# Kernel tuning notes

Measured on AMD Instinct MI355X. Metric: run time of the kernel, lower is better.

## Reference

```python
import jax, jax.numpy as jnp
import numpy as np
from jax import lax

RADII = (0.1, 0.2, 0.4)
NSAMPLES = (16, 32, 128)
MLPS = ((3, 32, 32, 64), (3, 64, 64, 128), (3, 64, 96, 128))  # divide_ratio=1


def fps(xyz, npoint):
    # iterative farthest point sampling; xyz [B,N,3] -> idx [B,npoint]
    B, N, _ = xyz.shape
    def body(carry, _):
        mind, last = carry
        p = jnp.take_along_axis(xyz, last[:, None, None], axis=1)  # [B,1,3]
        d = jnp.sum((xyz - p) ** 2, -1)
        mind = jnp.minimum(mind, d)
        nxt = jnp.argmax(mind, -1).astype(jnp.int32)
        return (mind, nxt), last
    init = (jnp.full((B, N), 1e10, xyz.dtype), jnp.zeros((B,), jnp.int32))
    _, idx = lax.scan(body, init, None, length=npoint)
    return jnp.transpose(idx)  # [B,npoint]


def ball_query(radius, nsample, xyz, new_xyz):
    # first-nsample neighbors within radius; pad with first valid index
    N = xyz.shape[1]
    sq = jnp.sum((new_xyz[:, :, None, :] - xyz[:, None, :, :]) ** 2, -1)  # [B,S,N]
    cand = jnp.where(sq < radius * radius,
                     jnp.arange(N, dtype=jnp.int32)[None, None, :], N)
    idx = jnp.sort(cand, axis=-1)[:, :, :nsample]
    first = idx[:, :, :1]
    return jnp.where(idx == N, first, idx).astype(jnp.int32)


def scale_branch(xyz, new_xyz, radius, nsample, weights):
    idx = ball_query(radius, nsample, xyz, new_xyz)
    grouped = jax.vmap(lambda x, i: x[i])(xyz, idx)          # [B,S,ns,3]
    h = grouped - new_xyz[:, :, None, :]                      # relative coords (points=None)
    for w, b in weights:                                      # shared 1x1-conv MLP
        h = jax.nn.relu(jnp.einsum('bsnc,co->bsno', h, w) + b)
    return jnp.max(h, axis=2)                                 # maxpool over neighbors [B,S,C]


def _forward(pcd, params, wf, bf):
    npoint = pcd.shape[1] // 8
    idx = fps(pcd, npoint)
    new_xyz = jnp.take_along_axis(pcd, idx[:, :, None], axis=1)  # [B,S,3]
    feats = [scale_branch(pcd, new_xyz, RADII[i], NSAMPLES[i], params[i]) for i in range(3)]
    h = jnp.concatenate(feats, axis=-1)                          # [B,S,320]
    return jnp.einsum('bsc,co->bso', h, wf) + bf                 # patch values [B,S,1]


def setup_inputs() -> dict:
    key = jax.random.key(0)
    ks = jax.random.split(key, 32)
    B, N = 8, 4096
    inp = {"pcd": jax.random.uniform(ks[0], (B, N, 3), jnp.float32)}
    ki = 1
    for si, dims in enumerate(MLPS):
        for li in range(3):
            cin, cout = dims[li], dims[li + 1]
            inp[f"w{si}{li}"] = jax.random.normal(ks[ki], (cin, cout), jnp.float32) * (2.0 / cin) ** 0.5
            inp[f"b{si}{li}"] = jnp.zeros((cout,), jnp.float32)
            ki += 1
    inp["wf"] = jax.random.normal(ks[ki], (320, 1), jnp.float32) * 0.05
    inp["bf"] = jnp.zeros((1,), jnp.float32)
    return inp


def reference(pcd, w00, b00, w01, b01, w02, b02,
              w10, b10, w11, b11, w12, b12,
              w20, b20, w21, b21, w22, b22, wf, bf):
    params = [[(w00, b00), (w01, b01), (w02, b02)],
              [(w10, b10), (w11, b11), (w12, b12)],
              [(w20, b20), (w21, b21), (w22, b22)]]
    return _forward(pcd, params, wf, bf)
```

## Files before the change

### kernel.cpp

```cpp
#include <hip/hip_runtime.h>

#define BATCH 8
#define NPTS 4096
#define NSAMP 512

#define ROW_SHR(n) (0x110 | (n))
#define ROW_BCAST15 0x142
#define ROW_BCAST31 0x143

template <int CTRL, int RMASK>
__device__ __forceinline__ float fmax_dpp(float x) {
  int t = __builtin_amdgcn_update_dpp(0, __float_as_int(x), CTRL, RMASK, 0xf, true);
  return fmaxf(x, __int_as_float(t));
}

__device__ __forceinline__ float wave_max(float x) {
  x = fmax_dpp<ROW_SHR(1), 0xf>(x);
  x = fmax_dpp<ROW_SHR(2), 0xf>(x);
  x = fmax_dpp<ROW_SHR(4), 0xf>(x);
  x = fmax_dpp<ROW_SHR(8), 0xf>(x);
  x = fmax_dpp<ROW_BCAST15, 0xa>(x);
  x = fmax_dpp<ROW_BCAST31, 0xc>(x);
  return x;
}

__device__ __forceinline__ void tsec(int g, const float* __restrict__ w,
                                     float* __restrict__ wt, int cin, int cinp,
                                     int cout, int base) {
  int local = g - base;
  if (local < 0 || local >= cinp * cout) return;
  int oc = local / cinp, ic = local % cinp;
  wt[base + local] = (ic < cin) ? w[ic * cout + oc] : 0.0f;
}

__device__ __forceinline__ void rowpack(int g, const float* __restrict__ w20,
                                        const float* __restrict__ b20,
                                        const float* __restrict__ w21,
                                        float* __restrict__ wt, int base) {
  int local = g - base;
  if (local < 0 || local >= 4 * 64 * 32) return;
  int wq = local / (64 * 32);
  int r = local % (64 * 32);
  int k = r / 32, j = r % 32;
  float v;
  if (j < 3) v = w20[j * 64 + k];
  else if (j == 3) v = b20[k];
  else if (j < 28) v = w21[k * 96 + wq * 24 + (j - 4)];
  else v = 0.0f;
  wt[base + local] = v;
}

#define W00 0
#define W01 128
#define W02 1152
#define W10 3200
#define W11 3456
#define W12 7552
#define WROW 15744
#define W22V 23936
#define WT_TOTAL 36224

__global__ __launch_bounds__(256) void prep_kernel(
    const float* w00, const float* w01, const float* w02,
    const float* w10, const float* w11, const float* w12,
    const float* w20, const float* b20, const float* w21, const float* w22,
    float* __restrict__ wt) {
  int g = blockIdx.x * 256 + threadIdx.x;
  tsec(g, w00, wt, 3, 4, 32, W00);
  tsec(g, w01, wt, 32, 32, 32, W01);
  tsec(g, w02, wt, 32, 32, 64, W02);
  tsec(g, w10, wt, 3, 4, 64, W10);
  tsec(g, w11, wt, 64, 64, 64, W11);
  tsec(g, w12, wt, 64, 64, 128, W12);
  rowpack(g, w20, b20, w21, wt, WROW);
  tsec(g, w22, wt, 96, 96, 128, W22V);
}

template <int TOC, int TN>
__device__ __forceinline__ void ib(float (&acc)[TOC][TN], const float* bias) {
#pragma unroll
  for (int j = 0; j < TOC; ++j) {
    float bj = bias[j];
#pragma unroll
    for (int i = 0; i < TN; ++i) acc[j][i] = bj;
  }
}

template <int CIN4, int TOC, int TN, int NTPI, int WS>
__device__ __forceinline__ void layer_acc(const float* __restrict__ wtb,
                                          const float* hin,
                                          float (&acc)[TOC][TN], int tn) {
#pragma unroll 2
  for (int c4 = 0; c4 < CIN4; ++c4) {
    float hv[4][TN];
#pragma unroll
    for (int k = 0; k < 4; ++k) {
      const float* src = &hin[(c4 * 4 + k) * NTPI + tn * TN];
      if constexpr (TN == 1) {
        hv[k][0] = src[0];
      } else if constexpr (TN == 2) {
        float2 v = *(const float2*)src; hv[k][0] = v.x; hv[k][1] = v.y;
      } else {
        float4 v = *(const float4*)src;
        hv[k][0] = v.x; hv[k][1] = v.y; hv[k][2] = v.z; hv[k][3] = v.w;
      }
    }
#pragma unroll
    for (int j = 0; j < TOC; ++j) {
      float4 w4 = *(const float4*)&wtb[j * WS + c4 * 4];
#pragma unroll
      for (int i = 0; i < TN; ++i) {
        acc[j][i] = fmaf(hv[0][i], w4.x, acc[j][i]);
        acc[j][i] = fmaf(hv[1][i], w4.y, acc[j][i]);
        acc[j][i] = fmaf(hv[2][i], w4.z, acc[j][i]);
        acc[j][i] = fmaf(hv[3][i], w4.w, acc[j][i]);
      }
    }
  }
}

template <int TOC, int TN, int NTPO>
__device__ __forceinline__ void store_relu(float* hout,
                                           float (&acc)[TOC][TN], int tn) {
#pragma unroll
  for (int j = 0; j < TOC; ++j) {
    float* dst = &hout[j * NTPO + tn * TN];
    if constexpr (TN == 1) {
      dst[0] = fmaxf(acc[j][0], 0.0f);
    } else if constexpr (TN == 2) {
      *(float2*)dst = make_float2(fmaxf(acc[j][0], 0.0f),
                                  fmaxf(acc[j][1], 0.0f));
    } else {
      *(float4*)dst = make_float4(fmaxf(acc[j][0], 0.0f),
                                  fmaxf(acc[j][1], 0.0f),
                                  fmaxf(acc[j][2], 0.0f),
                                  fmaxf(acc[j][3], 0.0f));
    }
  }
}

template <int TOC, int TN>
__device__ __forceinline__ void rmax_upd(float (&r)[TOC],
                                         float (&acc)[TOC][TN]) {
#pragma unroll
  for (int j = 0; j < TOC; ++j) {
    float m = 0.0f;
#pragma unroll
    for (int i = 0; i < TN; ++i) m = fmaxf(m, acc[j][i]);
    r[j] = fmaxf(r[j], m);
  }
}

template <int TOC, int TN>
__device__ __forceinline__ float rmax_dot(const float* wfp,
                                          float (&acc)[TOC][TN], int tn) {
  float s = 0.0f;
#pragma unroll
  for (int j = 0; j < TOC; ++j) {
    float v = 0.0f;
#pragma unroll
    for (int i = 0; i < TN; ++i) v = fmaxf(v, acc[j][i]);
    v = fmaxf(v, __shfl_xor(v, 1));
    v = fmaxf(v, __shfl_xor(v, 2));
    v = fmaxf(v, __shfl_xor(v, 4));
    v = fmaxf(v, __shfl_xor(v, 8));
    if (tn == 0) s = fmaf(v, wfp[j], s);
  }
  return s;
}

__global__ __launch_bounds__(256) void fused_kernel(
    const float* __restrict__ pcd, float* __restrict__ new_xyz,
    int* __restrict__ ctrl, const float* __restrict__ wt,
    const float* __restrict__ b00, const float* __restrict__ b01,
    const float* __restrict__ b02, const float* __restrict__ b10,
    const float* __restrict__ b11, const float* __restrict__ b12,
    const float* __restrict__ b21, const float* __restrict__ b22,
    const float* __restrict__ wf, const float* __restrict__ bf,
    float* __restrict__ out) {
  __shared__ __align__(16) float lds[6160];

  const int tid = threadIdx.x;
  int* progress = ctrl + 8;

  if (tid == 0) ((int*)lds)[0] = atomicAdd(&ctrl[0], 1);
  __syncthreads();
  const int ticket = ((int*)lds)[0];

  if (ticket < BATCH) {
    const int b = ticket;
    const int t = tid;
    const int wave = t >> 6, lane = t & 63;
    const float* xb = pcd + (size_t)b * NPTS * 3;
    float4* slot = (float4*)(lds + 16);

    float X[16], Y[16], Z[16], mind[16];
    {
      float f[48];
      float4* vv = (float4*)f;
      const float4* src = (const float4*)xb + t * 12;
#pragma unroll
      for (int q = 0; q < 12; ++q) vv[q] = src[q];
#pragma unroll
      for (int j = 0; j < 16; ++j) {
        X[j] = f[3 * j + 0]; Y[j] = f[3 * j + 1]; Z[j] = f[3 * j + 2];
        mind[j] = 10000000000.0f;
      }
    }
    float px = xb[0], py = xb[1], pz = xb[2];

    for (int it = 0; it < NSAMP; ++it) {
      if (t == 0) {
        int* dst = (int*)(new_xyz + ((size_t)b * NSAMP + it) * 3);
        atomicExch(&dst[0], __float_as_int(px));
        atomicExch(&dst[1], __float_as_int(py));
        atomicExch(&dst[2], __float_as_int(pz));
        if ((it & 7) == 7)
          __hip_atomic_store(&progress[b], it + 1, __ATOMIC_RELEASE,
                             __HIP_MEMORY_SCOPE_AGENT);
      }
      float bv = -1.0f, bx = 0.0f, by = 0.0f, bz = 0.0f;
#pragma unroll
      for (int j = 0; j < 16; ++j) {
        float dx = __fsub_rn(X[j], px);
        float dy = __fsub_rn(Y[j], py);
        float dz = __fsub_rn(Z[j], pz);
        float d = __fadd_rn(__fadd_rn(__fmul_rn(dx, dx), __fmul_rn(dy, dy)),
                            __fmul_rn(dz, dz));
        float m = fminf(mind[j], d);
        mind[j] = m;
        bool g = m > bv;
        bv = g ? m : bv;
        bx = g ? X[j] : bx; by = g ? Y[j] : by; bz = g ? Z[j] : bz;
      }
      float wmax = __int_as_float(
          __builtin_amdgcn_readlane(__float_as_int(wave_max(bv)), 63));
      unsigned long long msk = __ballot(bv == wmax);
      if (lane == __ffsll(msk) - 1)
        slot[(it & 1) * 4 + wave] = make_float4(bx, by, bz, wmax);
      __syncthreads();
      float4 cur = slot[(it & 1) * 4 + 0];
#pragma unroll
      for (int w = 1; w < 4; ++w) {
        float4 sw = slot[(it & 1) * 4 + w];
        if (sw.w > cur.w) cur = sw;
      }
      px = cur.x; py = cur.y; pz = cur.z;
    }
    return;
  }

  const int tk = ticket - BATCH;
  const int b = tk & 7;
  const int s = tk >> 3;
  const int bs = (b << 9) | s;
  const int lane = tid & 63;
  const int wave = tid >> 6;
  const int tn = tid & 15, toc = tid >> 4;
  const float* xb = pcd + (size_t)b * NPTS * 3;

  float* bc = lds + 4;
  float* wsum = lds + 8;
  float* h2 = lds + 16;
  unsigned long long* masks = (unsigned long long*)(lds + 16);
  unsigned short* gl = (unsigned short*)(lds + 400);
  float* cbuf = lds + 488;
  float* sB = lds + 760;
  float* sA = lds + 2936;

  if (tid == 0) {
    while (__hip_atomic_load(&progress[b], __ATOMIC_ACQUIRE,
                             __HIP_MEMORY_SCOPE_AGENT) <= s)
      __builtin_amdgcn_s_sleep(2);
    const int* src = (const int*)(new_xyz + (size_t)bs * 3);
    bc[0] = __int_as_float(__hip_atomic_load(&src[0], __ATOMIC_RELAXED,
                                             __HIP_MEMORY_SCOPE_AGENT));
    bc[1] = __int_as_float(__hip_atomic_load(&src[1], __ATOMIC_RELAXED,
                                             __HIP_MEMORY_SCOPE_AGENT));
    bc[2] = __int_as_float(__hip_atomic_load(&src[2], __ATOMIC_RELAXED,
                                             __HIP_MEMORY_SCOPE_AGENT));
  }
  __syncthreads();
  const float cx = bc[0], cy = bc[1], cz = bc[2];

  const float r2a = (float)(0.1 * 0.1);
  const float r2b = (float)(0.2 * 0.2);
  const float r2c = (float)(0.4 * 0.4);
#pragma unroll 4
  for (int j = 0; j < 16; ++j) {
    int i = (j << 8) | tid;
    const float* p = xb + i * 3;
    float dx = __fsub_rn(cx, p[0]);
    float dy = __fsub_rn(cy, p[1]);
    float dz = __fsub_rn(cz, p[2]);
    float sq = __fadd_rn(__fadd_rn(__fmul_rn(dx, dx), __fmul_rn(dy, dy)),
                         __fmul_rn(dz, dz));
    unsigned long long m0 = __ballot(sq < r2a);
    unsigned long long m1 = __ballot(sq < r2b);
    unsigned long long m2 = __ballot(sq < r2c);
    if (lane == 0) {
      int c = (j << 2) | wave;
      masks[0 * 64 + c] = m0; masks[1 * 64 + c] = m1; masks[2 * 64 + c] = m2;
    }
  }
  __syncthreads();

  if (wave < 3) {
    const int ns  = (wave == 0) ? 16 : (wave == 1) ? 32 : 128;
    const int off = (wave == 0) ? 0  : (wave == 1) ? 16 : 48;
    unsigned long long m = masks[wave * 64 + lane];
    int pc = (int)__popcll(m);
    int incl = pc;
#pragma unroll
    for (int o = 1; o < 64; o <<= 1) {
      int u = __shfl_up(incl, o);
      if (lane >= o) incl += u;
    }
    int ex = incl - pc;
    int total = __shfl(incl, 63);
    unsigned short* glw = gl + off;
    unsigned long long mm = m;
    int p = ex;
    while (mm && p < ns) {
      int l = (int)__builtin_ctzll(mm);
      mm &= mm - 1;
      glw[p++] = (unsigned short)((lane << 6) | l);
    }
    int cnt = total < ns ? total : ns;
    unsigned long long nz = __ballot(pc > 0);
    int fl = __ffsll(nz) - 1;
    int myf = (lane << 6) | (int)__builtin_ctzll(m | 0x8000000000000000ull);
    int fidx = __shfl(myf, fl);
    for (int k = cnt + lane; k < ns; k += 64) glw[k] = (unsigned short)fidx;
  }
  __syncthreads();

  const int gi0 = gl[48 + lane];
  const int gi1 = gl[112 + lane];
  if (tid < 68) cbuf[3 * 68 + tid] = 0.0f;
  if (tid < 48) {
    int j = gl[tid];
    const float* p = xb + 3 * j;
    cbuf[0 * 68 + tid] = __fsub_rn(p[0], cx);
    cbuf[1 * 68 + tid] = __fsub_rn(p[1], cy);
    cbuf[2 * 68 + tid] = __fsub_rn(p[2], cz);
  }
  const float* q0 = xb + 3 * gi0;
  const float* q1 = xb + 3 * gi1;
  const float dx0 = __fsub_rn(q0[0], cx);
  const float dy0 = __fsub_rn(q0[1], cy);
  const float dz0 = __fsub_rn(q0[2], cz);
  const float dx1 = __fsub_rn(q1[0], cx);
  const float dy1 = __fsub_rn(q1[1], cy);
  const float dz1 = __fsub_rn(q1[2], cz);
  __syncthreads();

  const int wq = __builtin_amdgcn_readfirstlane(wave);
  float dot = 0.0f;

  {
    float a[2][1]; ib<2, 1>(a, b00 + toc * 2);
    layer_acc<1, 2, 1, 68, 4>(wt + W00 + (toc * 2) * 4, cbuf, a, tn);
    store_relu<2, 1, 18>(sB + (toc * 2) * 18, a, tn);
  }
  __syncthreads();

  {
    float a[2][1]; ib<2, 1>(a, b01 + toc * 2);
    layer_acc<8, 2, 1, 18, 32>(wt + W01 + (toc * 2) * 32, sB, a, tn);
    store_relu<2, 1, 18>(sA + (toc * 2) * 18, a, tn);
  }
  __syncthreads();

  {
    float a[4][1]; ib<4, 1>(a, b02 + toc * 4);
    layer_acc<8, 4, 1, 18, 32>(wt + W02 + (toc * 4) * 32, sA, a, tn);
    dot += rmax_dot<4, 1>(wf + toc * 4, a, tn);
    float a1[4][2]; ib<4, 2>(a1, b10 + toc * 4);
    layer_acc<1, 4, 2, 68, 4>(wt + W10 + (toc * 4) * 4, cbuf + 16, a1, tn);
    store_relu<4, 2, 34>(sB + (toc * 4) * 34, a1, tn);
  }
  __syncthreads();

  {
    float a[4][2]; ib<4, 2>(a, b11 + toc * 4);
    layer_acc<16, 4, 2, 34, 64>(wt + W11 + (toc * 4) * 64, sB, a, tn);
    store_relu<4, 2, 34>(sA + (toc * 4) * 34, a, tn);
  }
  __syncthreads();

  {
    float a[8][2]; ib<8, 2>(a, b12 + toc * 8);
    layer_acc<16, 8, 2, 34, 64>(wt + W12 + (toc * 8) * 64, sA, a, tn);
    dot += rmax_dot<8, 2>(wf + 64 + toc * 8, a, tn);
  }
  __syncthreads();

  float rm2[8];
#pragma unroll
  for (int j = 0; j < 8; ++j) rm2[j] = 0.0f;

  {
    const float* wp = wt + WROW + wq * 2048;
    const float* bp = b21 + wq * 24;
    float acc[24];
#pragma unroll
    for (int j = 0; j < 24; ++j) acc[j] = bp[j];
#pragma unroll 4
    for (int k = 0; k < 64; ++k) {
      const float* row = wp + k * 32;
      float a2 = row[3];
      a2 = fmaf(dx0, row[0], a2);
      a2 = fmaf(dy0, row[1], a2);
      a2 = fmaf(dz0, row[2], a2);
      float hv = fmaxf(a2, 0.0f);
#pragma unroll
      for (int j = 0; j < 24; ++j) acc[j] = fmaf(hv, row[4 + j], acc[j]);
    }
#pragma unroll
    for (int j = 0; j < 24; ++j)
      h2[(wq * 24 + j) * 64 + lane] = fmaxf(acc[j], 0.0f);
  }
  __syncthreads();

  {
    float a[8][4]; ib<8, 4>(a, b22 + toc * 8);
    layer_acc<24, 8, 4, 64, 96>(wt + W22V + (toc * 8) * 96, h2, a, tn);
    rmax_upd<8, 4>(rm2, a);
  }
  __syncthreads();

  {
    const float* wp = wt + WROW + wq * 2048;
    const float* bp = b21 + wq * 24;
    float acc[24];
#pragma unroll
    for (int j = 0; j < 24; ++j) acc[j] = bp[j];
#pragma unroll 4
    for (int k = 0; k < 64; ++k) {
      const float* row = wp + k * 32;
      float a2 = row[3];
      a2 = fmaf(dx1, row[0], a2);
      a2 = fmaf(dy1, row[1], a2);
      a2 = fmaf(dz1, row[2], a2);
      float hv = fmaxf(a2, 0.0f);
#pragma unroll
      for (int j = 0; j < 24; ++j) acc[j] = fmaf(hv, row[4 + j], acc[j]);
    }
#pragma unroll
    for (int j = 0; j < 24; ++j)
      h2[(wq * 24 + j) * 64 + lane] = fmaxf(acc[j], 0.0f);
  }
  __syncthreads();

  {
    float a[8][4]; ib<8, 4>(a, b22 + toc * 8);
    layer_acc<24, 8, 4, 64, 96>(wt + W22V + (toc * 8) * 96, h2, a, tn);
    rmax_upd<8, 4>(rm2, a);
#pragma unroll
    for (int j = 0; j < 8; ++j) {
      float v = rm2[j];
      v = fmaxf(v, __shfl_xor(v, 1));
      v = fmaxf(v, __shfl_xor(v, 2));
      v = fmaxf(v, __shfl_xor(v, 4));
      v = fmaxf(v, __shfl_xor(v, 8));
      if (tn == 0) dot = fmaf(v, wf[192 + toc * 8 + j], dot);
    }
  }

#pragma unroll
  for (int o = 1; o < 64; o <<= 1) dot += __shfl_xor(dot, o);
  if (lane == 0) wsum[wq] = dot;
  __syncthreads();
  if (tid == 0)
    out[bs] = wsum[0] + wsum[1] + wsum[2] + wsum[3] + bf[0];
}

extern "C" void kernel_launch(void* const* d_in, const int* in_sizes, int n_in,
                              void* d_out, int out_size, void* d_ws, size_t ws_size,
                              hipStream_t stream) {
  const float* pcd = (const float*)d_in[0];
  float* wsf = (float*)d_ws;
  float* new_xyz = wsf;
  float* wt = wsf + 12288;
  int* ctrl = (int*)(wsf + 48512);

  hipMemsetAsync(ctrl, 0, 64, stream);

  prep_kernel<<<(WT_TOTAL + 255) / 256, 256, 0, stream>>>(
      (const float*)d_in[1], (const float*)d_in[3], (const float*)d_in[5],
      (const float*)d_in[7], (const float*)d_in[9], (const float*)d_in[11],
      (const float*)d_in[13], (const float*)d_in[14], (const float*)d_in[15],
      (const float*)d_in[17], wt);

  fused_kernel<<<BATCH * NSAMP + BATCH, 256, 0, stream>>>(
      pcd, new_xyz, ctrl, wt,
      (const float*)d_in[2],  (const float*)d_in[4],  (const float*)d_in[6],
      (const float*)d_in[8],  (const float*)d_in[10], (const float*)d_in[12],
      (const float*)d_in[16], (const float*)d_in[18],
      (const float*)d_in[19], (const float*)d_in[20],
      (float*)d_out);
}
```

Before: 599.9 us.

## Run scale-2 last MLP layer on bf16x3 MFMA with swizzled LDS

Replaces the FP32 scalar FMA loop for the third branch's 96->128 layer with MFMA 16x16x32 bf16 instructions. Precision is kept by splitting both weights and activations into hi/lo bf16 pairs and summing three products. Weights are pre-split and laid out in MFMA fragment order by the prep kernel. Activations are written to LDS in an XOR-swizzled bf16 layout to avoid bank conflicts. The two duplicated passes are folded into one loop, and the change adds conversion work plus a small accuracy risk from the split-bf16 scheme.

```diff
diff --git a/kernel.cpp b/kernel.cpp
--- a/kernel.cpp
+++ b/kernel.cpp
@@ -7,6 +7,18 @@
 #define ROW_SHR(n) (0x110 | (n))
 #define ROW_BCAST15 0x142
 #define ROW_BCAST31 0x143
+
+typedef __attribute__((ext_vector_type(8))) short bf16x8;
+typedef __attribute__((ext_vector_type(4))) float f32x4;
+
+__device__ __forceinline__ unsigned short f2bf(float f) {
+  unsigned u = __float_as_uint(f);
+  unsigned r = (u + 0x7FFFu + ((u >> 16) & 1u)) >> 16;
+  return (unsigned short)r;
+}
+__device__ __forceinline__ float bf2f(unsigned short h) {
+  return __uint_as_float(((unsigned)h) << 16);
+}
 
 template <int CTRL, int RMASK>
 __device__ __forceinline__ float fmax_dpp(float x) {
@@ -50,6 +62,24 @@
   wt[base + local] = v;
 }
 
+__device__ __forceinline__ void awfill(int g, const float* __restrict__ w22,
+                                       unsigned short* __restrict__ aw,
+                                       int base) {
+  int id = g - base;
+  if (id < 0 || id >= 12288) return;
+  int e = id & 7;
+  int l = (id >> 3) & 63;
+  int bq = id >> 9;
+  int ot = bq / 3, ks = bq % 3;
+  int oc = ot * 16 + (l & 15);
+  int k = ks * 32 + (l >> 4) * 8 + e;
+  float v = w22[k * 128 + oc];
+  unsigned short h = f2bf(v);
+  unsigned short lo = f2bf(__fsub_rn(v, bf2f(h)));
+  aw[(bq * 64 + l) * 16 + e] = h;
+  aw[(bq * 64 + l) * 16 + 8 + e] = lo;
+}
+
 #define W00 0
 #define W01 128
 #define W02 1152
@@ -57,14 +87,14 @@
 #define W11 3456
 #define W12 7552
 #define WROW 15744
-#define W22V 23936
-#define WT_TOTAL 36224
+#define AWID 23936
+#define ID_TOTAL 36224
 
 __global__ __launch_bounds__(256) void prep_kernel(
     const float* w00, const float* w01, const float* w02,
     const float* w10, const float* w11, const float* w12,
     const float* w20, const float* b20, const float* w21, const float* w22,
-    float* __restrict__ wt) {
+    float* __restrict__ wt, unsigned short* __restrict__ aw) {
   int g = blockIdx.x * 256 + threadIdx.x;
   tsec(g, w00, wt, 3, 4, 32, W00);
   tsec(g, w01, wt, 32, 32, 32, W01);
@@ -73,7 +103,7 @@
   tsec(g, w11, wt, 64, 64, 64, W11);
   tsec(g, w12, wt, 64, 64, 128, W12);
   rowpack(g, w20, b20, w21, wt, WROW);
-  tsec(g, w22, wt, 96, 96, 128, W22V);
+  awfill(g, w22, aw, AWID);
 }
 
 template <int TOC, int TN>
@@ -140,18 +170,6 @@
 }
 
 template <int TOC, int TN>
-__device__ __forceinline__ void rmax_upd(float (&r)[TOC],
-                                         float (&acc)[TOC][TN]) {
-#pragma unroll
-  for (int j = 0; j < TOC; ++j) {
-    float m = 0.0f;
-#pragma unroll
-    for (int i = 0; i < TN; ++i) m = fmaxf(m, acc[j][i]);
-    r[j] = fmaxf(r[j], m);
-  }
-}
-
-template <int TOC, int TN>
 __device__ __forceinline__ float rmax_dot(const float* wfp,
                                           float (&acc)[TOC][TN], int tn) {
   float s = 0.0f;
@@ -172,6 +190,7 @@
 __global__ __launch_bounds__(256) void fused_kernel(
     const float* __restrict__ pcd, float* __restrict__ new_xyz,
     int* __restrict__ ctrl, const float* __restrict__ wt,
+    const unsigned short* __restrict__ aw,
     const float* __restrict__ b00, const float* __restrict__ b01,
     const float* __restrict__ b02, const float* __restrict__ b10,
     const float* __restrict__ b11, const float* __restrict__ b12,
@@ -261,7 +280,7 @@
 
   float* bc = lds + 4;
   float* wsum = lds + 8;
-  float* h2 = lds + 16;
+  char* h2b = (char*)(lds + 16);
   unsigned long long* masks = (unsigned long long*)(lds + 16);
   unsigned short* gl = (unsigned short*)(lds + 400);
   float* cbuf = lds + 488;
@@ -399,74 +418,119 @@
   float rm2[8];
 #pragma unroll
   for (int j = 0; j < 8; ++j) rm2[j] = 0.0f;
-
-  {
-    const float* wp = wt + WROW + wq * 2048;
-    const float* bp = b21 + wq * 24;
-    float acc[24];
-#pragma unroll
-    for (int j = 0; j < 24; ++j) acc[j] = bp[j];
+  const int fq = lane >> 4, fr = lane & 15;
+
+#pragma unroll 1
+  for (int pass = 0; pass < 2; ++pass) {
+    const float pdx = pass ? dx1 : dx0;
+    const float pdy = pass ? dy1 : dy0;
+    const float pdz = pass ? dz1 : dz0;
+
+    {
+      const float* wp = wt + WROW + wq * 2048;
+      const float* bp = b21 + wq * 24;
+      float acc[24];
+#pragma unroll
+      for (int j = 0; j < 24; ++j) acc[j] = bp[j];
 #pragma unroll 4
-    for (int k = 0; k < 64; ++k) {
-      const float* row = wp + k * 32;
-      float a2 = row[3];
-      a2 = fmaf(dx0, row[0], a2);
-      a2 = fmaf(dy0, row[1], a2);
-      a2 = fmaf(dz0, row[2], a2);
-      float hv = fmaxf(a2, 0.0f);
-#pragma unroll
-      for (int j = 0; j < 24; ++j) acc[j] = fmaf(hv, row[4 + j], acc[j]);
-    }
-#pragma unroll
-    for (int j = 0; j < 24; ++j)
-      h2[(wq * 24 + j) * 64 + lane] = fmaxf(acc[j], 0.0f);
-  }
-  __syncthreads();
-
-  {
-    float a[8][4]; ib<8, 4>(a, b22 + toc * 8);
-    layer_acc<24, 8, 4, 64, 96>(wt + W22V + (toc * 8) * 96, h2, a, tn);
-    rmax_upd<8, 4>(rm2, a);
-  }
-  __syncthreads();
-
-  {
-    const float* wp = wt + WROW + wq * 2048;
-    const float* bp = b21 + wq * 24;
-    float acc[24];
-#pragma unroll
-    for (int j = 0; j < 24; ++j) acc[j] = bp[j];
-#pragma unroll 4
-    for (int k = 0; k < 64; ++k) {
-      const float* row = wp + k * 32;
-      float a2 = row[3];
-      a2 = fmaf(dx1, row[0], a2);
-      a2 = fmaf(dy1, row[1], a2);
-      a2 = fmaf(dz1, row[2], a2);
-      float hv = fmaxf(a2, 0.0f);
-#pragma unroll
-      for (int j = 0; j < 24; ++j) acc[j] = fmaf(hv, row[4 + j], acc[j]);
-    }
-#pragma unroll
-    for (int j = 0; j < 24; ++j)
-      h2[(wq * 24 + j) * 64 + lane] = fmaxf(acc[j], 0.0f);
-  }
-  __syncthreads();
-
-  {
-    float a[8][4]; ib<8, 4>(a, b22 + toc * 8);
-    layer_acc<24, 8, 4, 64, 96>(wt + W22V + (toc * 8) * 96, h2, a, tn);
-    rmax_upd<8, 4>(rm2, a);
-#pragma unroll
-    for (int j = 0; j < 8; ++j) {
-      float v = rm2[j];
+      for (int k = 0; k < 64; ++k) {
+        const float* row = wp + k * 32;
+        float a2 = row[3];
+        a2 = fmaf(pdx, row[0], a2);
+        a2 = fmaf(pdy, row[1], a2);
+        a2 = fmaf(pdz, row[2], a2);
+        float hv = fmaxf(a2, 0.0f);
+#pragma unroll
+        for (int j = 0; j < 24; ++j) acc[j] = fmaf(hv, row[4 + j], acc[j]);
+      }
+      char* hb = h2b + lane * 384;
+      const int nx = lane & 7;
+#pragma unroll
+      for (int c = 0; c < 3; ++c) {
+        int ph[4], pl[4];
+#pragma unroll
+        for (int q = 0; q < 4; ++q) {
+          float a0 = fmaxf(acc[c * 8 + 2 * q], 0.0f);
+          float a1 = fmaxf(acc[c * 8 + 2 * q + 1], 0.0f);
+          unsigned short h0 = f2bf(a0);
+          unsigned short l0 = f2bf(__fsub_rn(a0, bf2f(h0)));
+          unsigned short h1 = f2bf(a1);
+          unsigned short l1 = f2bf(__fsub_rn(a1, bf2f(h1)));
+          ph[q] = (int)((unsigned)h0 | ((unsigned)h1 << 16));
+          pl[q] = (int)((unsigned)l0 | ((unsigned)l1 << 16));
+        }
+        const int g = 6 * wq + 2 * c;
+        *(int4*)(hb + ((g ^ nx) << 4)) = make_int4(ph[0], ph[1], ph[2], ph[3]);
+        *(int4*)(hb + (((g + 1) ^ nx) << 4)) =
+            make_int4(pl[0], pl[1], pl[2], pl[3]);
+      }
+    }
+    __syncthreads();
+
+    {
+      f32x4 C[2][4];
+#pragma unroll
+      for (int i = 0; i < 2; ++i) {
+        float bv[4];
+#pragma unroll
+        for (int r = 0; r < 4; ++r)
+          bv[r] = b22[(wq * 2 + i) * 16 + fq * 4 + r];
+#pragma unroll
+        for (int t = 0; t < 4; ++t)
+#pragma unroll
+          for (int r = 0; r < 4; ++r) C[i][t][r] = bv[r];
+      }
+#pragma unroll
+      for (int ks = 0; ks < 3; ++ks) {
+        bf16x8 Ah[2], Al[2];
+#pragma unroll
+        for (int i = 0; i < 2; ++i) {
+          const unsigned short* ab =
+              aw + (((wq * 2 + i) * 3 + ks) * 64 + lane) * 16;
+          Ah[i] = *(const bf16x8*)ab;
+          Al[i] = *(const bf16x8*)(ab + 8);
+        }
+        const int kc = ks * 4 + fq;
+#pragma unroll
+        for (int t = 0; t < 4; ++t) {
+          const int n = t * 16 + fr, nx = n & 7;
+          const char* nb = h2b + n * 384;
+          bf16x8 Bh = *(const bf16x8*)(nb + (((2 * kc) ^ nx) << 4));
+          bf16x8 Bl = *(const bf16x8*)(nb + (((2 * kc + 1) ^ nx) << 4));
+#pragma unroll
+          for (int i = 0; i < 2; ++i) {
+            C[i][t] = __builtin_amdgcn_mfma_f32_16x16x32_bf16(
+                Ah[i], Bh, C[i][t], 0, 0, 0);
+            C[i][t] = __builtin_amdgcn_mfma_f32_16x16x32_bf16(
+                Ah[i], Bl, C[i][t], 0, 0, 0);
+            C[i][t] = __builtin_amdgcn_mfma_f32_16x16x32_bf16(
+                Al[i], Bh, C[i][t], 0, 0, 0);
+          }
+        }
+      }
+#pragma unroll
+      for (int i = 0; i < 2; ++i)
+#pragma unroll
+        for (int t = 0; t < 4; ++t)
+#pragma unroll
+          for (int r = 0; r < 4; ++r)
+            rm2[i * 4 + r] = fmaxf(rm2[i * 4 + r], fmaxf(C[i][t][r], 0.0f));
+    }
+    __syncthreads();
+  }
+
+#pragma unroll
+  for (int i = 0; i < 2; ++i)
+#pragma unroll
+    for (int r = 0; r < 4; ++r) {
+      float v = rm2[i * 4 + r];
       v = fmaxf(v, __shfl_xor(v, 1));
       v = fmaxf(v, __shfl_xor(v, 2));
       v = fmaxf(v, __shfl_xor(v, 4));
       v = fmaxf(v, __shfl_xor(v, 8));
-      if (tn == 0) dot = fmaf(v, wf[192 + toc * 8 + j], dot);
-    }
-  }
+      if (fr == 0)
+        dot = fmaf(v, wf[192 + (wq * 2 + i) * 16 + fq * 4 + r], dot);
+    }
 
 #pragma unroll
   for (int o = 1; o < 64; o <<= 1) dot += __shfl_xor(dot, o);
@@ -483,18 +547,19 @@
   float* wsf = (float*)d_ws;
   float* new_xyz = wsf;
   float* wt = wsf + 12288;
+  unsigned short* aw = (unsigned short*)(wsf + 36224);
   int* ctrl = (int*)(wsf + 48512);
 
   hipMemsetAsync(ctrl, 0, 64, stream);
 
-  prep_kernel<<<(WT_TOTAL + 255) / 256, 256, 0, stream>>>(
+  prep_kernel<<<(ID_TOTAL + 255) / 256, 256, 0, stream>>>(
       (const float*)d_in[1], (const float*)d_in[3], (const float*)d_in[5],
       (const float*)d_in[7], (const float*)d_in[9], (const float*)d_in[11],
       (const float*)d_in[13], (const float*)d_in[14], (const float*)d_in[15],
-      (const float*)d_in[17], wt);
+      (const float*)d_in[17], wt, aw);
 
   fused_kernel<<<BATCH * NSAMP + BATCH, 256, 0, stream>>>(
-      pcd, new_xyz, ctrl, wt,
+      pcd, new_xyz, ctrl, wt, aw,
       (const float*)d_in[2],  (const float*)d_in[4],  (const float*)d_in[6],
       (const float*)d_in[8],  (const float*)d_in[10], (const float*)d_in[12],
       (const float*)d_in[16], (const float*)d_in[18],
```

After: 483.9 us, median of 2. 1.24x faster.
